# Kernel tuning notes

Measured on AMD Instinct MI355X. Metric: run time of the kernel, lower is better.

The kernel has to match this reference:

```python
import jax, jax.numpy as jnp
import numpy as np

B, T, D = 2, 2048, 1024
H, W = 16, 256  # n_head, window_size
HD = D // H


def setup_inputs() -> dict:
    key = jax.random.key(0)
    ks = jax.random.split(key, 5)
    s = 0.02
    return {
        "x": jax.random.normal(ks[0], (B, T, D), dtype=jnp.float32),
        "Wqkv": jax.random.normal(ks[1], (3 * D, D), dtype=jnp.float32) * s,
        "bqkv": jax.random.normal(ks[2], (3 * D,), dtype=jnp.float32) * s,
        "Wo": jax.random.normal(ks[3], (D, D), dtype=jnp.float32) * s,
        "bo": jax.random.normal(ks[4], (D,), dtype=jnp.float32) * s,
    }


def reference(x, Wqkv, bqkv, Wo, bo):
    b, t, d = x.shape
    qkv = x @ Wqkv.T + bqkv  # [b, t, 3d]
    # rearrange 'b t (c h d) -> c b h t d'
    qkv = qkv.reshape(b, t, 3, H, HD)
    q = jnp.transpose(qkv[:, :, 0], (0, 2, 1, 3))  # [b, h, t, hd]
    k = jnp.transpose(qkv[:, :, 1], (0, 2, 1, 3))
    v = jnp.transpose(qkv[:, :, 2], (0, 2, 1, 3))
    scores = jnp.einsum('bhid,bhjd->bhij', q, k) / jnp.sqrt(jnp.float32(HD))
    i = jnp.arange(t)[:, None]
    j = jnp.arange(t)[None, :]
    # tril(diag=0) & triu(diag=-(W-1)): j <= i and j >= i - (W-1)
    mask = (j <= i) & (j >= i - (W - 1))
    scores = jnp.where(mask, scores, -jnp.inf)
    probs = jax.nn.softmax(scores, axis=-1)
    y = jnp.einsum('bhij,bhjd->bhid', probs, v)
    y = jnp.transpose(y, (0, 2, 1, 3)).reshape(b, t, d)  # b h t d -> b t (h d)
    return y @ Wo.T + bo
```

## Files before the change

kernel.cpp:

```cpp
#include <hip/hip_runtime.h>
#include <hip/hip_bf16.h>
#include <stdint.h>


typedef __attribute__((ext_vector_type(8))) short short8;
typedef __attribute__((ext_vector_type(4))) float f32x4;

#define MFMA16(a, b, c) __builtin_amdgcn_mfma_f32_16x16x32_bf16((a), (b), (c), 0, 0, 0)

static __device__ __forceinline__ void gl_lds16(const void* g, void* l) {
  __builtin_amdgcn_global_load_lds(
      (const __attribute__((address_space(1))) unsigned int*)g,
      (__attribute__((address_space(3))) unsigned int*)l, 16, 0, 0);
}

#define LGKM0 do { asm volatile("s_waitcnt lgkmcnt(0)" ::: "memory"); \
                   __builtin_amdgcn_sched_barrier(0); } while (0)
#define BARM do { asm volatile("" ::: "memory"); \
                  __builtin_amdgcn_s_barrier(); \
                  asm volatile("" ::: "memory"); } while (0)

static __device__ __forceinline__ uint32_t pkbf(float x, float y) {
  union { __hip_bfloat16 h; uint16_t u; } a, b;
  a.h = __float2bfloat16(x);
  b.h = __float2bfloat16(y);
  return (uint32_t)a.u | ((uint32_t)b.u << 16);
}

__global__ void cvt_all(const float* __restrict__ x, const float* __restrict__ wqkv,
                        const float* __restrict__ wo, __hip_bfloat16* __restrict__ xb,
                        __hip_bfloat16* __restrict__ wqkvb,
                        __hip_bfloat16* __restrict__ wob) {
  const int N0 = 524288, N1 = 393216, N2 = 131072;
  int i = blockIdx.x * blockDim.x + threadIdx.x;
  const int stride = gridDim.x * blockDim.x;
  for (; i < N0 + N1 + N2; i += stride) {
    const float* in;
    __hip_bfloat16* out;
    int gidx;
    if (i < N0) { in = x; out = xb; gidx = i; }
    else if (i < N0 + N1) { in = wqkv; out = wqkvb; gidx = i - N0; }
    else { in = wo; out = wob; gidx = i - N0 - N1; }
    const float4* p = (const float4*)in + (size_t)gidx * 2;
    float4 v0 = p[0], v1 = p[1];
    union { short8 s; __hip_bfloat16 h[8]; } u;
    u.h[0] = __float2bfloat16(v0.x); u.h[1] = __float2bfloat16(v0.y);
    u.h[2] = __float2bfloat16(v0.z); u.h[3] = __float2bfloat16(v0.w);
    u.h[4] = __float2bfloat16(v1.x); u.h[5] = __float2bfloat16(v1.y);
    u.h[6] = __float2bfloat16(v1.z); u.h[7] = __float2bfloat16(v1.w);
    ((short8*)out)[gidx] = u.s;
  }
}

__global__ __launch_bounds__(512) void gemm_qkv(
    const __hip_bfloat16* __restrict__ A, const __hip_bfloat16* __restrict__ Bm,
    const float* __restrict__ bias,
    __hip_bfloat16* __restrict__ qb, __hip_bfloat16* __restrict__ kb,
    __hip_bfloat16* __restrict__ vt2) {
  __shared__ alignas(128) char smem[114688];
  const int tid = threadIdx.x;
  const int lane = tid & 63, w = tid >> 6;
  const int wm = w >> 2, wn = w & 3;
  const int r = lane & 15, g = lane >> 4;
  const int K = 1024, NT = 16;

  const int cpx = gridDim.x >> 3;
  const int swzb = (blockIdx.x & 7) * cpx + (blockIdx.x >> 3);
  const int bm = swzb >> 4, bn = swzb & 15;

  const int srow = tid >> 3;
  const int e = (tid & 7) ^ ((tid >> 4) & 7);
  const int koff = (e >> 2) * 32 + (e & 3) * 8;
  const __hip_bfloat16* aU[4];
  const __hip_bfloat16* bU[3];
#pragma unroll
  for (int U = 0; U < 4; ++U)
    aU[U] = A + (size_t)(bm * 256 + U * 64 + srow) * K + koff;
#pragma unroll
  for (int U = 0; U < 3; ++U)
    bU[U] = Bm + (size_t)(bn * 192 + U * 64 + srow) * K + koff;
  const int ldst = tid * 16;

#define STA(t, U) gl_lds16(aU[U] + (t) * 64, smem + ((t) & 1) * 57344 + (U) * 8192 + ldst)
#define STB(t, U) gl_lds16(bU[U] + (t) * 64, smem + ((t) & 1) * 57344 + 32768 + (U) * 8192 + ldst)

  const int hsw = (r >> 1) & 7;
  const int s0 = ((0 + g) ^ hsw) * 16;
  const int s1 = ((4 + g) ^ hsw) * 16;
  const int rdA = (wm * 128 + r) * 128;
  const int rdB = 32768 + (wn * 48 + r) * 128;

  f32x4 acc[8][3] = {};
  short8 a0[4][2], a1[4][2], bb[3][2];

#pragma unroll
  for (int U = 0; U < 4; ++U) STA(0, U);
#pragma unroll
  for (int U = 0; U < 3; ++U) STB(0, U);
#pragma unroll
  for (int U = 0; U < 4; ++U) STA(1, U);
#pragma unroll
  for (int U = 0; U < 3; ++U) STB(1, U);
  asm volatile("s_waitcnt vmcnt(7)" ::: "memory");
  BARM;

#pragma unroll 1
  for (int t = 0; t < NT; ++t) {
    const char* cb = smem + (t & 1) * 57344;
#pragma unroll
    for (int i = 0; i < 4; ++i) {
      a0[i][0] = *(const short8*)(cb + rdA + i * 2048 + s0);
      a0[i][1] = *(const short8*)(cb + rdA + i * 2048 + s1);
    }
#pragma unroll
    for (int j = 0; j < 2; ++j) {
      bb[j][0] = *(const short8*)(cb + rdB + j * 2048 + s0);
      bb[j][1] = *(const short8*)(cb + rdB + j * 2048 + s1);
    }
    BARM;
    LGKM0;
    __builtin_amdgcn_s_setprio(1);
#pragma unroll
    for (int i = 0; i < 4; ++i)
#pragma unroll
      for (int j = 0; j < 2; ++j) acc[i][j] = MFMA16(a0[i][0], bb[j][0], acc[i][j]);
#pragma unroll
    for (int i = 0; i < 4; ++i)
#pragma unroll
      for (int j = 0; j < 2; ++j) acc[i][j] = MFMA16(a0[i][1], bb[j][1], acc[i][j]);
    __builtin_amdgcn_s_setprio(0);
    BARM;
#pragma unroll
    for (int i = 0; i < 4; ++i) {
      a1[i][0] = *(const short8*)(cb + rdA + (i + 4) * 2048 + s0);
      a1[i][1] = *(const short8*)(cb + rdA + (i + 4) * 2048 + s1);
    }
    BARM;
    LGKM0;
    __builtin_amdgcn_s_setprio(1);
#pragma unroll
    for (int i = 0; i < 4; ++i)
#pragma unroll
      for (int j = 0; j < 2; ++j) acc[i + 4][j] = MFMA16(a1[i][0], bb[j][0], acc[i + 4][j]);
#pragma unroll
    for (int i = 0; i < 4; ++i)
#pragma unroll
      for (int j = 0; j < 2; ++j) acc[i + 4][j] = MFMA16(a1[i][1], bb[j][1], acc[i + 4][j]);
    __builtin_amdgcn_s_setprio(0);
    BARM;
    bb[2][0] = *(const short8*)(cb + rdB + 2 * 2048 + s0);
    bb[2][1] = *(const short8*)(cb + rdB + 2 * 2048 + s1);
    if (t + 2 < NT) {
      STA(t + 2, 0); STA(t + 2, 1); STA(t + 2, 2); STA(t + 2, 3);
    }
    BARM;
    LGKM0;
    __builtin_amdgcn_s_setprio(1);
#pragma unroll
    for (int i = 0; i < 4; ++i) acc[i + 4][2] = MFMA16(a1[i][0], bb[2][0], acc[i + 4][2]);
#pragma unroll
    for (int i = 0; i < 4; ++i) acc[i + 4][2] = MFMA16(a1[i][1], bb[2][1], acc[i + 4][2]);
    __builtin_amdgcn_s_setprio(0);
    BARM;
    if (t + 2 < NT) {
      STB(t + 2, 0); STB(t + 2, 1); STB(t + 2, 2);
    }
    BARM;
    __builtin_amdgcn_s_setprio(1);
#pragma unroll
    for (int i = 0; i < 4; ++i) acc[i][2] = MFMA16(a0[i][0], bb[2][0], acc[i][2]);
#pragma unroll
    for (int i = 0; i < 4; ++i) acc[i][2] = MFMA16(a0[i][1], bb[2][1], acc[i][2]);
    __builtin_amdgcn_s_setprio(0);
    if (t + 2 < NT) {
      asm volatile("s_waitcnt vmcnt(7)" ::: "memory");
    } else if (t + 1 < NT) {
      asm volatile("s_waitcnt vmcnt(0)" ::: "memory");
    }
    BARM;
  }
#undef STA
#undef STB

  float bjv[3];
  const int nb = bn * 192 + wn * 48;
#pragma unroll
  for (int j = 0; j < 3; ++j) bjv[j] = bias[nb + j * 16 + r];
#pragma unroll
  for (int i = 0; i < 8; ++i) {
    const int m0 = bm * 256 + wm * 128 + i * 16 + g * 4;
#pragma unroll
    for (int j = 0; j < 3; ++j) {
      const int nn = nb + j * 16 + r;
      const int c = nn >> 10, h = (nn >> 6) & 15, hd = nn & 63;
      const int b_ = m0 >> 11, t0 = m0 & 2047;
      const size_t hb = (size_t)(b_ * 16 + h);
      if (c == 0) {
#pragma unroll
        for (int q = 0; q < 4; ++q)
          qb[(hb * 2048 + t0 + q) * 64 + hd] =
              __float2bfloat16((acc[i][j][q] + bjv[j]) * 0.125f);
      } else if (c == 1) {
#pragma unroll
        for (int q = 0; q < 4; ++q)
          kb[(hb * 2048 + t0 + q) * 64 + hd] =
              __float2bfloat16(acc[i][j][q] + bjv[j]);
      } else {
        union { uint2 u; __hip_bfloat16 hh[4]; } pk;
#pragma unroll
        for (int q = 0; q < 4; ++q)
          pk.hh[q] = __float2bfloat16(acc[i][j][q] + bjv[j]);
        const int kk = t0 & 31;
        const int pp = ((kk & 12) << 1) + ((kk & 16) >> 2);
        *(uint2*)&vt2[hb * 131072 + (size_t)(t0 >> 5) * 2048 + hd * 32 + pp] =
            pk.u;
      }
    }
  }
}

__global__ __launch_bounds__(512, 4) void gemm_out8(
    const __hip_bfloat16* __restrict__ A, const __hip_bfloat16* __restrict__ Bm,
    const float* __restrict__ bias, float* __restrict__ outF) {
  __shared__ alignas(128) char smem[65536];
  const int tid = threadIdx.x;
  const int lane = tid & 63, w = tid >> 6;
  const int wm = w >> 2, wn = w & 3;
  const int r = lane & 15, g = lane >> 4;
  const int K = 1024, NT = 16;

  const int cpx = gridDim.x >> 3;
  const int swzb = (blockIdx.x & 7) * cpx + (blockIdx.x >> 3);
  const int bm = swzb >> 3, bn = swzb & 7;

  const int srow = tid >> 3;
  const int e = (tid & 7) ^ ((tid >> 4) & 7);
  const int koff = (e >> 2) * 32 + (e & 3) * 8;
  const __hip_bfloat16* aU[2];
  const __hip_bfloat16* bU[2];
#pragma unroll
  for (int U = 0; U < 2; ++U) {
    aU[U] = A + (size_t)(bm * 128 + U * 64 + srow) * K + koff;
    bU[U] = Bm + (size_t)(bn * 128 + U * 64 + srow) * K + koff;
  }
  const int ldst = tid * 16;

#define STA(t, U) gl_lds16(aU[U] + (t) * 64, smem + ((t) & 1) * 32768 + (U) * 8192 + ldst)
#define STB(t, U) gl_lds16(bU[U] + (t) * 64, smem + ((t) & 1) * 32768 + 16384 + (U) * 8192 + ldst)

  const int hsw = (r >> 1) & 7;
  const int s0 = ((0 + g) ^ hsw) * 16;
  const int s1 = ((4 + g) ^ hsw) * 16;
  const int rdA = (wm * 64 + r) * 128;
  const int rdB = 16384 + (wn * 32 + r) * 128;

  f32x4 acc[4][2] = {};
  short8 af[4][2], bf[2][2];

  STA(0, 0); STA(0, 1); STB(0, 0); STB(0, 1);
  STA(1, 0); STA(1, 1); STB(1, 0); STB(1, 1);
  asm volatile("s_waitcnt vmcnt(4)" ::: "memory");
  BARM;

#pragma unroll 1
  for (int t = 0; t < NT; ++t) {
    const char* cb = smem + (t & 1) * 32768;
#pragma unroll
    for (int i = 0; i < 2; ++i) {
      af[i][0] = *(const short8*)(cb + rdA + i * 2048 + s0);
      af[i][1] = *(const short8*)(cb + rdA + i * 2048 + s1);
    }
#pragma unroll
    for (int j = 0; j < 2; ++j) {
      bf[j][0] = *(const short8*)(cb + rdB + j * 2048 + s0);
      bf[j][1] = *(const short8*)(cb + rdB + j * 2048 + s1);
    }
    BARM;
    LGKM0;
    __builtin_amdgcn_s_setprio(1);
#pragma unroll
    for (int i = 0; i < 2; ++i)
#pragma unroll
      for (int j = 0; j < 2; ++j) acc[i][j] = MFMA16(af[i][0], bf[j][0], acc[i][j]);
#pragma unroll
    for (int i = 0; i < 2; ++i)
#pragma unroll
      for (int j = 0; j < 2; ++j) acc[i][j] = MFMA16(af[i][1], bf[j][1], acc[i][j]);
    __builtin_amdgcn_s_setprio(0);
    BARM;
#pragma unroll
    for (int i = 0; i < 2; ++i) {
      af[i + 2][0] = *(const short8*)(cb + rdA + (i + 2) * 2048 + s0);
      af[i + 2][1] = *(const short8*)(cb + rdA + (i + 2) * 2048 + s1);
    }
    if (t + 2 < NT) { STB(t + 2, 0); STB(t + 2, 1); }
    BARM;
    LGKM0;
    __builtin_amdgcn_s_setprio(1);
#pragma unroll
    for (int i = 0; i < 2; ++i)
#pragma unroll
      for (int j = 0; j < 2; ++j) acc[i + 2][j] = MFMA16(af[i + 2][0], bf[j][0], acc[i + 2][j]);
#pragma unroll
    for (int i = 0; i < 2; ++i)
#pragma unroll
      for (int j = 0; j < 2; ++j) acc[i + 2][j] = MFMA16(af[i + 2][1], bf[j][1], acc[i + 2][j]);
    __builtin_amdgcn_s_setprio(0);
    BARM;
    if (t + 2 < NT) {
      STA(t + 2, 0); STA(t + 2, 1);
      asm volatile("s_waitcnt vmcnt(4)" ::: "memory");
    } else if (t + 1 < NT) {
      asm volatile("s_waitcnt vmcnt(0)" ::: "memory");
    }
    BARM;
  }
#undef STA
#undef STB

  float bjv[2];
  const int nb = bn * 128 + wn * 32;
#pragma unroll
  for (int j = 0; j < 2; ++j) bjv[j] = bias[nb + j * 16 + r];
#pragma unroll
  for (int i = 0; i < 4; ++i) {
    const int m0 = bm * 128 + wm * 64 + i * 16 + g * 4;
#pragma unroll
    for (int j = 0; j < 2; ++j) {
      const int nn = nb + j * 16 + r;
#pragma unroll
      for (int q = 0; q < 4; ++q)
        outF[(size_t)(m0 + q) * 1024 + nn] = acc[i][j][q] + bjv[j];
    }
  }
}

__global__ __launch_bounds__(512, 2) void attn_local(
    const __hip_bfloat16* __restrict__ qb, const __hip_bfloat16* __restrict__ kb,
    const __hip_bfloat16* __restrict__ vt2, __hip_bfloat16* __restrict__ yb) {
  __shared__ alignas(16) char smem[49152];
  const int xcd = blockIdx.x & 7;
  const int idx = blockIdx.x >> 3;
  const int bh = xcd + (idx >> 4) * 8;
  const int qt = idx & 15;
  const int tid = threadIdx.x;
  const int w = tid >> 6, lane = tid & 63;
  const int r = lane & 15, g = lane >> 4;
  const int qa = qt * 128 + w * 16;

  const __hip_bfloat16* qp = qb + (size_t)bh * 2048 * 64;
  const __hip_bfloat16* kp = kb + (size_t)bh * 2048 * 64;
  const __hip_bfloat16* vpb = vt2 + (size_t)bh * 131072 + r * 32 + g * 8;

  const int t_lo = (qt >= 2) ? (4 * qt - 8) : 0;
  const int t_hi = 4 * qt + 3;
  const int nunits = (t_hi - t_lo + 1) << 8;
  short8 stg[6];
#pragma unroll
  for (int rr = 0; rr < 6; ++rr) {
    const int u = rr * 512 + tid;
    if (u < nunits) {
      const int tt = u >> 8, row = (u >> 3) & 31, sl = u & 7;
      stg[rr] = *(const short8*)&kp[(size_t)((t_lo + tt) * 32 + row) * 64 + sl * 8];
    }
  }
#pragma unroll
  for (int rr = 0; rr < 6; ++rr) {
    const int u = rr * 512 + tid;
    if (u < nunits) {
      const int tt = u >> 8, row = (u >> 3) & 31, sl = u & 7;
      *(short8*)(smem + tt * 4096 + row * 128 + ((sl ^ (row & 7)) << 4)) = stg[rr];
    }
  }
  __syncthreads();

  const short8 qf0 = *(const short8*)&qp[(qa + r) * 64 + g * 8];
  const short8 qf1 = *(const short8*)&qp[(qa + r) * 64 + g * 8 + 32];

  f32x4 acc[4] = {};
  float m = -1e30f;
  float lsum = 0.f;

  const int wlo = ((qa >= 256) ? ((qa - 255) >> 5) : 0) - t_lo;
  const int whi = ((qa + 15) >> 5) - t_lo;
  const int xsw = (r & 7) << 4;

#pragma unroll 1
  for (int tt = wlo; tt <= whi; ++tt) {
    const int tabs = t_lo + tt;
    const int kbase = tabs << 5;
    const short8 v0 = *(const short8*)(vpb + (size_t)tabs * 2048);
    const short8 v1 = *(const short8*)(vpb + (size_t)tabs * 2048 + 512);
    const short8 v2 = *(const short8*)(vpb + (size_t)tabs * 2048 + 1024);
    const short8 v3 = *(const short8*)(vpb + (size_t)tabs * 2048 + 1536);
    const char* kt = smem + tt * 4096;
    const short8 k00 = *(const short8*)(kt + r * 128 + (((g) << 4) ^ xsw));
    const short8 k01 = *(const short8*)(kt + r * 128 + (((4 + g) << 4) ^ xsw));
    const short8 k10 = *(const short8*)(kt + (16 + r) * 128 + (((g) << 4) ^ xsw));
    const short8 k11 = *(const short8*)(kt + (16 + r) * 128 + (((4 + g) << 4) ^ xsw));
    f32x4 st0 = {}, st1 = {};
    st0 = MFMA16(k00, qf0, st0);
    st0 = MFMA16(k01, qf1, st0);
    st1 = MFMA16(k10, qf0, st1);
    st1 = MFMA16(k11, qf1, st1);
    float sv[2][4];
#pragma unroll
    for (int q = 0; q < 4; ++q) {
      const unsigned d0 = (unsigned)(qa + r) - (unsigned)(kbase + g * 4 + q);
      const unsigned d1 = (unsigned)(qa + r) - (unsigned)(kbase + 16 + g * 4 + q);
      sv[0][q] = (d0 <= 255u) ? st0[q] : -1e30f;
      sv[1][q] = (d1 <= 255u) ? st1[q] : -1e30f;
    }
    const float tmax = fmaxf(
        fmaxf(fmaxf(sv[0][0], sv[0][1]), fmaxf(sv[0][2], sv[0][3])),
        fmaxf(fmaxf(sv[1][0], sv[1][1]), fmaxf(sv[1][2], sv[1][3])));
    if (!__all(tmax <= m + 8.f)) {
      float rm = tmax;
      rm = fmaxf(rm, __shfl_xor(rm, 16));
      rm = fmaxf(rm, __shfl_xor(rm, 32));
      const float mnew = fmaxf(m, rm);
      const float fac = __expf(m - mnew);
      m = mnew;
      lsum *= fac;
      acc[0] *= fac; acc[1] *= fac; acc[2] *= fac; acc[3] *= fac;
    }
    float p[2][4];
#pragma unroll
    for (int f = 0; f < 2; ++f)
#pragma unroll
      for (int q = 0; q < 4; ++q) {
        p[f][q] = __expf(sv[f][q] - m);
        lsum += p[f][q];
      }
    union { short8 s; uint32_t u[4]; } pb;
    pb.u[0] = pkbf(p[0][0], p[0][1]);
    pb.u[1] = pkbf(p[0][2], p[0][3]);
    pb.u[2] = pkbf(p[1][0], p[1][1]);
    pb.u[3] = pkbf(p[1][2], p[1][3]);
    acc[0] = MFMA16(v0, pb.s, acc[0]);
    acc[1] = MFMA16(v1, pb.s, acc[1]);
    acc[2] = MFMA16(v2, pb.s, acc[2]);
    acc[3] = MFMA16(v3, pb.s, acc[3]);
  }

  lsum += __shfl_xor(lsum, 16);
  lsum += __shfl_xor(lsum, 32);
  const float inv = 1.f / lsum;

  const int b_ = bh >> 4, h = bh & 15;
  __hip_bfloat16* yrow = yb + (size_t)(b_ * 2048 + qa + r) * 1024 + h * 64;
#pragma unroll
  for (int u = 0; u < 4; ++u) {
    union { uint2 uu; __hip_bfloat16 hh[4]; } pk;
#pragma unroll
    for (int q = 0; q < 4; ++q) pk.hh[q] = __float2bfloat16(acc[u][q] * inv);
    *(uint2*)&yrow[u * 16 + g * 4] = pk.uu;
  }
}

extern "C" void kernel_launch(void* const* d_in, const int* in_sizes, int n_in,
                              void* d_out, int out_size, void* d_ws,
                              size_t ws_size, hipStream_t stream) {
  const float* x = (const float*)d_in[0];
  const float* Wqkv = (const float*)d_in[1];
  const float* bqkv = (const float*)d_in[2];
  const float* Wo = (const float*)d_in[3];
  const float* bo = (const float*)d_in[4];
  float* out = (float*)d_out;

  char* ws = (char*)d_ws;
  __hip_bfloat16* xb = (__hip_bfloat16*)(ws + 0);
  __hip_bfloat16* wqkvb = (__hip_bfloat16*)(ws + 8388608);
  __hip_bfloat16* wob = (__hip_bfloat16*)(ws + 14680064);
  __hip_bfloat16* qb = (__hip_bfloat16*)(ws + 16777216);
  __hip_bfloat16* kb = (__hip_bfloat16*)(ws + 25165824);
  __hip_bfloat16* vt2 = (__hip_bfloat16*)(ws + 33554432);
  __hip_bfloat16* yb = (__hip_bfloat16*)(ws + 41943040);

  cvt_all<<<2048, 256, 0, stream>>>(x, Wqkv, Wo, xb, wqkvb, wob);

  gemm_qkv<<<256, 512, 0, stream>>>(xb, wqkvb, bqkv, qb, kb, vt2);
  attn_local<<<512, 512, 0, stream>>>(qb, kb, vt2, yb);
  gemm_out8<<<256, 512, 0, stream>>>(yb, wob, bo, out);
}
```

Before: 75.95 us.

## Halve QKV GEMM M-tile to 128 rows and double grid size

The QKV projection GEMM block tile shrinks from 256x192 to 128x192, so the grid goes from 256 to 512 blocks. LDS per block drops from 112 KB to 80 KB, and a launch-bounds occupancy hint is added so two blocks can share a CU. The per-iteration MFMA/LDS-read/prefetch schedule is rebuilt around the smaller tile, with fewer phases and an adjusted vmcnt wait. The aim is better latency hiding and balance across CUs, at the cost of more global re-reads of the weight matrix and less reuse per block.

```diff
diff --git a/kernel.cpp b/kernel.cpp
--- a/kernel.cpp
+++ b/kernel.cpp
@@ -52,12 +52,12 @@
   }
 }
 
-__global__ __launch_bounds__(512) void gemm_qkv(
+__global__ __launch_bounds__(512, 4) void gemm_qkv(
     const __hip_bfloat16* __restrict__ A, const __hip_bfloat16* __restrict__ Bm,
     const float* __restrict__ bias,
     __hip_bfloat16* __restrict__ qb, __hip_bfloat16* __restrict__ kb,
     __hip_bfloat16* __restrict__ vt2) {
-  __shared__ alignas(128) char smem[114688];
+  __shared__ alignas(128) char smem[81920];
   const int tid = threadIdx.x;
   const int lane = tid & 63, w = tid >> 6;
   const int wm = w >> 2, wn = w & 3;
@@ -71,109 +71,81 @@
   const int srow = tid >> 3;
   const int e = (tid & 7) ^ ((tid >> 4) & 7);
   const int koff = (e >> 2) * 32 + (e & 3) * 8;
-  const __hip_bfloat16* aU[4];
+  const __hip_bfloat16* aU[2];
   const __hip_bfloat16* bU[3];
 #pragma unroll
-  for (int U = 0; U < 4; ++U)
-    aU[U] = A + (size_t)(bm * 256 + U * 64 + srow) * K + koff;
+  for (int U = 0; U < 2; ++U)
+    aU[U] = A + (size_t)(bm * 128 + U * 64 + srow) * K + koff;
 #pragma unroll
   for (int U = 0; U < 3; ++U)
     bU[U] = Bm + (size_t)(bn * 192 + U * 64 + srow) * K + koff;
   const int ldst = tid * 16;
 
-#define STA(t, U) gl_lds16(aU[U] + (t) * 64, smem + ((t) & 1) * 57344 + (U) * 8192 + ldst)
-#define STB(t, U) gl_lds16(bU[U] + (t) * 64, smem + ((t) & 1) * 57344 + 32768 + (U) * 8192 + ldst)
+#define STA(t, U) gl_lds16(aU[U] + (t) * 64, smem + ((t) & 1) * 40960 + (U) * 8192 + ldst)
+#define STB(t, U) gl_lds16(bU[U] + (t) * 64, smem + ((t) & 1) * 40960 + 16384 + (U) * 8192 + ldst)
 
   const int hsw = (r >> 1) & 7;
   const int s0 = ((0 + g) ^ hsw) * 16;
   const int s1 = ((4 + g) ^ hsw) * 16;
-  const int rdA = (wm * 128 + r) * 128;
-  const int rdB = 32768 + (wn * 48 + r) * 128;
-
-  f32x4 acc[8][3] = {};
-  short8 a0[4][2], a1[4][2], bb[3][2];
-
-#pragma unroll
-  for (int U = 0; U < 4; ++U) STA(0, U);
-#pragma unroll
-  for (int U = 0; U < 3; ++U) STB(0, U);
-#pragma unroll
-  for (int U = 0; U < 4; ++U) STA(1, U);
-#pragma unroll
-  for (int U = 0; U < 3; ++U) STB(1, U);
-  asm volatile("s_waitcnt vmcnt(7)" ::: "memory");
+  const int rdA = (wm * 64 + r) * 128;
+  const int rdB = 16384 + (wn * 48 + r) * 128;
+
+  f32x4 acc[4][3] = {};
+  short8 af[4][2], bf[3][2];
+
+  STA(0, 0); STA(0, 1); STB(0, 0); STB(0, 1); STB(0, 2);
+  STA(1, 0); STA(1, 1); STB(1, 0); STB(1, 1); STB(1, 2);
+  asm volatile("s_waitcnt vmcnt(5)" ::: "memory");
   BARM;
 
 #pragma unroll 1
   for (int t = 0; t < NT; ++t) {
-    const char* cb = smem + (t & 1) * 57344;
-#pragma unroll
-    for (int i = 0; i < 4; ++i) {
-      a0[i][0] = *(const short8*)(cb + rdA + i * 2048 + s0);
-      a0[i][1] = *(const short8*)(cb + rdA + i * 2048 + s1);
-    }
-#pragma unroll
-    for (int j = 0; j < 2; ++j) {
-      bb[j][0] = *(const short8*)(cb + rdB + j * 2048 + s0);
-      bb[j][1] = *(const short8*)(cb + rdB + j * 2048 + s1);
+    const char* cb = smem + (t & 1) * 40960;
+#pragma unroll
+    for (int i = 0; i < 2; ++i) {
+      af[i][0] = *(const short8*)(cb + rdA + i * 2048 + s0);
+      af[i][1] = *(const short8*)(cb + rdA + i * 2048 + s1);
+    }
+#pragma unroll
+    for (int j = 0; j < 3; ++j) {
+      bf[j][0] = *(const short8*)(cb + rdB + j * 2048 + s0);
+      bf[j][1] = *(const short8*)(cb + rdB + j * 2048 + s1);
     }
     BARM;
     LGKM0;
     __builtin_amdgcn_s_setprio(1);
 #pragma unroll
-    for (int i = 0; i < 4; ++i)
-#pragma unroll
-      for (int j = 0; j < 2; ++j) acc[i][j] = MFMA16(a0[i][0], bb[j][0], acc[i][j]);
-#pragma unroll
-    for (int i = 0; i < 4; ++i)
-#pragma unroll
-      for (int j = 0; j < 2; ++j) acc[i][j] = MFMA16(a0[i][1], bb[j][1], acc[i][j]);
+    for (int i = 0; i < 2; ++i)
+#pragma unroll
+      for (int j = 0; j < 3; ++j) acc[i][j] = MFMA16(af[i][0], bf[j][0], acc[i][j]);
+#pragma unroll
+    for (int i = 0; i < 2; ++i)
+#pragma unroll
+      for (int j = 0; j < 3; ++j) acc[i][j] = MFMA16(af[i][1], bf[j][1], acc[i][j]);
     __builtin_amdgcn_s_setprio(0);
     BARM;
 #pragma unroll
-    for (int i = 0; i < 4; ++i) {
-      a1[i][0] = *(const short8*)(cb + rdA + (i + 4) * 2048 + s0);
-      a1[i][1] = *(const short8*)(cb + rdA + (i + 4) * 2048 + s1);
-    }
+    for (int i = 0; i < 2; ++i) {
+      af[i + 2][0] = *(const short8*)(cb + rdA + (i + 2) * 2048 + s0);
+      af[i + 2][1] = *(const short8*)(cb + rdA + (i + 2) * 2048 + s1);
+    }
+    if (t + 2 < NT) { STB(t + 2, 0); STB(t + 2, 1); STB(t + 2, 2); }
     BARM;
     LGKM0;
     __builtin_amdgcn_s_setprio(1);
 #pragma unroll
-    for (int i = 0; i < 4; ++i)
-#pragma unroll
-      for (int j = 0; j < 2; ++j) acc[i + 4][j] = MFMA16(a1[i][0], bb[j][0], acc[i + 4][j]);
-#pragma unroll
-    for (int i = 0; i < 4; ++i)
-#pragma unroll
-      for (int j = 0; j < 2; ++j) acc[i + 4][j] = MFMA16(a1[i][1], bb[j][1], acc[i + 4][j]);
+    for (int i = 0; i < 2; ++i)
+#pragma unroll
+      for (int j = 0; j < 3; ++j) acc[i + 2][j] = MFMA16(af[i + 2][0], bf[j][0], acc[i + 2][j]);
+#pragma unroll
+    for (int i = 0; i < 2; ++i)
+#pragma unroll
+      for (int j = 0; j < 3; ++j) acc[i + 2][j] = MFMA16(af[i + 2][1], bf[j][1], acc[i + 2][j]);
     __builtin_amdgcn_s_setprio(0);
     BARM;
-    bb[2][0] = *(const short8*)(cb + rdB + 2 * 2048 + s0);
-    bb[2][1] = *(const short8*)(cb + rdB + 2 * 2048 + s1);
     if (t + 2 < NT) {
-      STA(t + 2, 0); STA(t + 2, 1); STA(t + 2, 2); STA(t + 2, 3);
-    }
-    BARM;
-    LGKM0;
-    __builtin_amdgcn_s_setprio(1);
-#pragma unroll
-    for (int i = 0; i < 4; ++i) acc[i + 4][2] = MFMA16(a1[i][0], bb[2][0], acc[i + 4][2]);
-#pragma unroll
-    for (int i = 0; i < 4; ++i) acc[i + 4][2] = MFMA16(a1[i][1], bb[2][1], acc[i + 4][2]);
-    __builtin_amdgcn_s_setprio(0);
-    BARM;
-    if (t + 2 < NT) {
-      STB(t + 2, 0); STB(t + 2, 1); STB(t + 2, 2);
-    }
-    BARM;
-    __builtin_amdgcn_s_setprio(1);
-#pragma unroll
-    for (int i = 0; i < 4; ++i) acc[i][2] = MFMA16(a0[i][0], bb[2][0], acc[i][2]);
-#pragma unroll
-    for (int i = 0; i < 4; ++i) acc[i][2] = MFMA16(a0[i][1], bb[2][1], acc[i][2]);
-    __builtin_amdgcn_s_setprio(0);
-    if (t + 2 < NT) {
-      asm volatile("s_waitcnt vmcnt(7)" ::: "memory");
+      STA(t + 2, 0); STA(t + 2, 1);
+      asm volatile("s_waitcnt vmcnt(5)" ::: "memory");
     } else if (t + 1 < NT) {
       asm volatile("s_waitcnt vmcnt(0)" ::: "memory");
     }
@@ -187,8 +159,8 @@
 #pragma unroll
   for (int j = 0; j < 3; ++j) bjv[j] = bias[nb + j * 16 + r];
 #pragma unroll
-  for (int i = 0; i < 8; ++i) {
-    const int m0 = bm * 256 + wm * 128 + i * 16 + g * 4;
+  for (int i = 0; i < 4; ++i) {
+    const int m0 = bm * 128 + wm * 64 + i * 16 + g * 4;
 #pragma unroll
     for (int j = 0; j < 3; ++j) {
       const int nn = nb + j * 16 + r;
@@ -479,7 +451,7 @@
 
   cvt_all<<<2048, 256, 0, stream>>>(x, Wqkv, Wo, xb, wqkvb, wob);
 
-  gemm_qkv<<<256, 512, 0, stream>>>(xb, wqkvb, bqkv, qb, kb, vt2);
+  gemm_qkv<<<512, 512, 0, stream>>>(xb, wqkvb, bqkv, qb, kb, vt2);
   attn_local<<<512, 512, 0, stream>>>(qb, kb, vt2, yb);
   gemm_out8<<<256, 512, 0, stream>>>(yb, wob, bo, out);
 }
```

Result: faster. 72.11 us (-5.0%).
